# Kernel optimization log

Hardware: AMD Instinct MI355X
Metric: run time of the kernel (lower is better)

## Reference

```python
import jax, jax.numpy as jnp
import numpy as np

NUM_EMBEDDINGS = 1024
EMBEDDING_DIM = 256
COMMITMENT_COST = 0.25
DECAY = 0.99
EPSILON = 1e-05


def setup_inputs() -> dict:
    key = jax.random.key(0)
    k1, k2, k3 = jax.random.split(key, 3)
    z_e = jax.random.normal(k1, (32, 32, 32, EMBEDDING_DIM), dtype=jnp.float32)
    embedding = jax.random.normal(k2, (NUM_EMBEDDINGS, EMBEDDING_DIM), dtype=jnp.float32)
    ema_cluster_size = jnp.zeros((NUM_EMBEDDINGS,), dtype=jnp.float32)
    ema_w = jax.random.normal(k3, (NUM_EMBEDDINGS, EMBEDDING_DIM), dtype=jnp.float32)
    return {"z_e": z_e, "embedding": embedding,
            "ema_cluster_size": ema_cluster_size, "ema_w": ema_w}


def reference(z_e, embedding, ema_cluster_size, ema_w):
    K, D = embedding.shape
    flat = z_e.reshape(-1, D)  # [N, D]
    distances = (jnp.sum(flat * flat, axis=1, keepdims=True)
                 - 2.0 * (flat @ embedding.T)
                 + jnp.sum(embedding * embedding, axis=1))
    encoding_indices = jnp.argmin(distances, axis=1)  # [N]
    # one_hot @ embedding == gather of nearest codes
    z_q = embedding[encoding_indices].reshape(z_e.shape)

    # EMA codebook update (training branch, torch no_grad)
    counts = jax.ops.segment_sum(jnp.ones_like(encoding_indices, dtype=flat.dtype),
                                 encoding_indices, num_segments=K)  # encodings.sum(0)
    dw = jax.ops.segment_sum(flat, encoding_indices, num_segments=K)  # encodings.T @ flat
    new_cluster_size = DECAY * ema_cluster_size + (1.0 - DECAY) * counts
    new_ema_w = DECAY * ema_w + (1.0 - DECAY) * dw
    n = jnp.sum(new_cluster_size)
    cluster_size = (new_cluster_size + EPSILON) / (n + K * EPSILON) * n
    new_embedding = new_ema_w / cluster_size[:, None]

    codebook_loss = jnp.mean((z_q - jax.lax.stop_gradient(z_e)) ** 2)
    commitment_loss = COMMITMENT_COST * jnp.mean((z_e - jax.lax.stop_gradient(z_q)) ** 2)
    vq_loss = codebook_loss + commitment_loss
    z_q_st = z_e + jax.lax.stop_gradient(z_q - z_e)  # straight-through
    return (z_q_st, vq_loss, encoding_indices,
            new_embedding, new_cluster_size, new_ema_w)
```

## Files before the change

### kernel.cpp

```cpp
#include <hip/hip_runtime.h>

#define DECAY_F 0.99f
#define OMD_F   0.01f
#define EPS_F   1e-5f

typedef __attribute__((ext_vector_type(8)))  __bf16 bf16x8;
typedef __attribute__((ext_vector_type(16))) float  f32x16;

#define WSB_CNTI     0
#define WSB_LOSS     4096
#define WSB_DWACC    8192
#define WSB_CSUM     1056768
#define WSB_ENORM    1056832
#define WSB_IDX      1060928
#define WSB_EHI      1192000
#define WSB_ELO      1716288
#define WSB_SORT     2240576
#define WSB_CURS     2371648

#define OUT_ZQ    0
#define OUT_LOSS  8388608
#define OUT_IDX   8388609
#define OUT_EMB   8421377
#define OUT_CS    8683521
#define OUT_EMAW  8684545

__device__ __forceinline__ unsigned short f2bf(float x) {
    unsigned u = __builtin_bit_cast(unsigned, x);
    u += 0x7fffu + ((u >> 16) & 1u);
    return (unsigned short)(u >> 16);
}
__device__ __forceinline__ float bf2f(unsigned short h) {
    return __builtin_bit_cast(float, (unsigned)h << 16);
}
__device__ __forceinline__ void split8(const float4 a, const float4 b,
                                       uint4& hi, uint4& lo) {
    float f[8] = {a.x, a.y, a.z, a.w, b.x, b.y, b.z, b.w};
    unsigned short h[8], l[8];
    #pragma unroll
    for (int i = 0; i < 8; ++i) {
        h[i] = f2bf(f[i]);
        l[i] = f2bf(f[i] - bf2f(h[i]));
    }
    hi.x = (unsigned)h[0] | ((unsigned)h[1] << 16);
    hi.y = (unsigned)h[2] | ((unsigned)h[3] << 16);
    hi.z = (unsigned)h[4] | ((unsigned)h[5] << 16);
    hi.w = (unsigned)h[6] | ((unsigned)h[7] << 16);
    lo.x = (unsigned)l[0] | ((unsigned)l[1] << 16);
    lo.y = (unsigned)l[2] | ((unsigned)l[3] << 16);
    lo.z = (unsigned)l[4] | ((unsigned)l[5] << 16);
    lo.w = (unsigned)l[6] | ((unsigned)l[7] << 16);
}

__device__ __forceinline__ void load_lds16(const void* g, void* l) {
    __builtin_amdgcn_global_load_lds(
        (const __attribute__((address_space(1))) unsigned int*)g,
        (__attribute__((address_space(3))) unsigned int*)l, 16, 0, 0);
}

__global__ __launch_bounds__(256)
void esplit_enorm_kernel(const float* __restrict__ emb,
                         unsigned short* __restrict__ e_hi,
                         unsigned short* __restrict__ e_lo,
                         float* __restrict__ enorm,
                         float* __restrict__ dwacc,
                         int* __restrict__ cnt,
                         float* __restrict__ lossbuf) {
    const int tid = threadIdx.x, lane = tid & 63, wv = tid >> 6;
    const int gthread = blockIdx.x * 256 + tid;
    *(float4*)(dwacc + (size_t)gthread * 4) = make_float4(0.f, 0.f, 0.f, 0.f);
    if (gthread < 1024) cnt[gthread] = 0;
    if (gthread < 256)  lossbuf[gthread] = 0.f;

    const int k = blockIdx.x * 4 + wv;
    const float4 v = *(const float4*)(emb + (size_t)k * 256 + lane * 4);
    float f[4] = {v.x, v.y, v.z, v.w};
    unsigned short h[4], l[4];
    #pragma unroll
    for (int i = 0; i < 4; ++i) { h[i] = f2bf(f[i]); l[i] = f2bf(f[i] - bf2f(h[i])); }
    uint2 hi, lo;
    hi.x = (unsigned)h[0] | ((unsigned)h[1] << 16);
    hi.y = (unsigned)h[2] | ((unsigned)h[3] << 16);
    lo.x = (unsigned)l[0] | ((unsigned)l[1] << 16);
    lo.y = (unsigned)l[2] | ((unsigned)l[3] << 16);
    *(uint2*)(e_hi + (size_t)k * 256 + lane * 4) = hi;
    *(uint2*)(e_lo + (size_t)k * 256 + lane * 4) = lo;
    float s = v.x * v.x + v.y * v.y + v.z * v.z + v.w * v.w;
    #pragma unroll
    for (int off = 32; off > 0; off >>= 1) s += __shfl_down(s, off);
    if (lane == 0) enorm[k] = s;
}

__global__ __launch_bounds__(256, 2)
void argmin_kernel(const float* __restrict__ z,
                   const unsigned short* __restrict__ e_hi,
                   const unsigned short* __restrict__ e_lo,
                   const float* __restrict__ enorm,
                   const float* __restrict__ emb,
                   int* __restrict__ idx, float* __restrict__ idxf,
                   float* __restrict__ out_zq, int* __restrict__ cnt) {
    __shared__ unsigned short Ah[64 * 32], Al[64 * 32];
    __shared__ unsigned short Bh[256 * 32], Bl[256 * 32];

    const int tid  = threadIdx.x;
    const int lane = tid & 63;
    const int wv   = tid >> 6;
    const int l31  = lane & 31, lh = lane >> 5;
    const int row0 = blockIdx.x * 64;

    const int rA = tid >> 2, gA = tid & 3;
    const float* zA = z + (size_t)(row0 + rA) * 256 + gA * 8;
    const int offA = rA * 32 + ((gA ^ ((rA >> 1) & 3)) << 3);

    int gBoff[4], lBoff[4];
    #pragma unroll
    for (int i = 0; i < 4; ++i) {
        const int s = i * 256 + wv * 64 + lane;
        const int c = s >> 2, gp = s & 3;
        const int gl = gp ^ ((c >> 1) & 3);
        gBoff[i] = c * 256 + gl * 8;
        lBoff[i] = (i * 256 + wv * 64) * 8;
    }

    int offAf[2][2], offBf[2][2];
    #pragma unroll
    for (int i = 0; i < 2; ++i) {
        const int rt = i * 32 + l31;
        #pragma unroll
        for (int kk = 0; kk < 2; ++kk)
            offAf[i][kk] = rt * 32 + (((kk * 2 + lh) ^ ((rt >> 1) & 3)) << 3);
    }
    #pragma unroll
    for (int j = 0; j < 2; ++j) {
        const int cb = wv * 64 + j * 32 + l31;
        #pragma unroll
        for (int kk = 0; kk < 2; ++kk)
            offBf[j][kk] = cb * 32 + (((kk * 2 + lh) ^ ((cb >> 1) & 3)) << 3);
    }

    f32x16 acc[2][2];
    #pragma unroll
    for (int i = 0; i < 2; ++i)
        #pragma unroll
        for (int j = 0; j < 2; ++j) acc[i][j] = (f32x16)0.0f;

    float bestd[2][16];
    int   besti[2][16];
    #pragma unroll
    for (int i = 0; i < 2; ++i)
        #pragma unroll
        for (int r = 0; r < 16; ++r) { bestd[i][r] = 3.4e38f; besti[i][r] = 0; }

    float4 pA[2];
    auto prefA = [&](int kc_) {
        const int o = kc_ * 32;
        pA[0] = *(const float4*)(zA + o);
        pA[1] = *(const float4*)(zA + o + 4);
    };
    prefA(0);

    for (int csp = 0; csp < 4; ++csp) {
        const int ebase = csp * 65536;

        for (int kc = 0; kc < 8; ++kc) {
            __syncthreads();
            {
                uint4 h0, l0;
                split8(pA[0], pA[1], h0, l0);
                *(uint4*)(Ah + offA) = h0; *(uint4*)(Al + offA) = l0;
            }
            #pragma unroll
            for (int i = 0; i < 4; ++i) {
                load_lds16(e_hi + ebase + gBoff[i] + kc * 32, Bh + lBoff[i]);
                load_lds16(e_lo + ebase + gBoff[i] + kc * 32, Bl + lBoff[i]);
            }
            __syncthreads();
            if (kc < 7) prefA(kc + 1);
            else if (csp < 3) prefA(0);

            #pragma unroll
            for (int kk = 0; kk < 2; ++kk) {
                bf16x8 ah[2], al[2], bh[2], bl[2];
                #pragma unroll
                for (int i = 0; i < 2; ++i) {
                    ah[i] = __builtin_bit_cast(bf16x8, *(const uint4*)(Ah + offAf[i][kk]));
                    al[i] = __builtin_bit_cast(bf16x8, *(const uint4*)(Al + offAf[i][kk]));
                }
                #pragma unroll
                for (int j = 0; j < 2; ++j) {
                    bh[j] = __builtin_bit_cast(bf16x8, *(const uint4*)(Bh + offBf[j][kk]));
                    bl[j] = __builtin_bit_cast(bf16x8, *(const uint4*)(Bl + offBf[j][kk]));
                }
                #pragma unroll
                for (int j = 0; j < 2; ++j)
                    #pragma unroll
                    for (int i = 0; i < 2; ++i)
                        acc[i][j] = __builtin_amdgcn_mfma_f32_32x32x16_bf16(ah[i], bh[j], acc[i][j], 0, 0, 0);
                #pragma unroll
                for (int j = 0; j < 2; ++j)
                    #pragma unroll
                    for (int i = 0; i < 2; ++i)
                        acc[i][j] = __builtin_amdgcn_mfma_f32_32x32x16_bf16(al[i], bh[j], acc[i][j], 0, 0, 0);
                #pragma unroll
                for (int j = 0; j < 2; ++j)
                    #pragma unroll
                    for (int i = 0; i < 2; ++i)
                        acc[i][j] = __builtin_amdgcn_mfma_f32_32x32x16_bf16(ah[i], bl[j], acc[i][j], 0, 0, 0);
            }
        }

        #pragma unroll
        for (int j = 0; j < 2; ++j) {
            const int col = csp * 256 + wv * 64 + j * 32 + l31;
            const float en = enorm[col];
            #pragma unroll
            for (int i = 0; i < 2; ++i)
                #pragma unroll
                for (int r = 0; r < 16; ++r) {
                    const float d = fmaf(-2.0f, acc[i][j][r], en);
                    if (d < bestd[i][r] || (d == bestd[i][r] && col < besti[i][r])) {
                        bestd[i][r] = d; besti[i][r] = col;
                    }
                }
        }
        #pragma unroll
        for (int i = 0; i < 2; ++i)
            #pragma unroll
            for (int j = 0; j < 2; ++j) acc[i][j] = (f32x16)0.0f;
    }

    #pragma unroll
    for (int m = 1; m < 32; m <<= 1) {
        #pragma unroll
        for (int i = 0; i < 2; ++i)
            #pragma unroll
            for (int r = 0; r < 16; ++r) {
                const float od = __shfl_xor(bestd[i][r], m);
                const int   oi = __shfl_xor(besti[i][r], m);
                if (od < bestd[i][r] || (od == bestd[i][r] && oi < besti[i][r])) {
                    bestd[i][r] = od; besti[i][r] = oi;
                }
            }
    }

    __syncthreads();
    float* mg_d = (float*)Ah;
    int*   mg_i = (int*)Ah + 256;
    if (l31 == 0) {
        #pragma unroll
        for (int i = 0; i < 2; ++i)
            #pragma unroll
            for (int r = 0; r < 16; ++r) {
                const int rloc = i * 32 + (r & 3) + 8 * (r >> 2) + 4 * lh;
                mg_d[wv * 64 + rloc] = bestd[i][r];
                mg_i[wv * 64 + rloc] = besti[i][r];
            }
    }
    __syncthreads();
    if (tid < 64) {
        float d0 = mg_d[tid];
        int   i0 = mg_i[tid];
        #pragma unroll
        for (int w = 1; w < 4; ++w) {
            const float dw = mg_d[w * 64 + tid];
            const int   iw = mg_i[w * 64 + tid];
            if (dw < d0 || (dw == d0 && iw < i0)) { d0 = dw; i0 = iw; }
        }
        const int n = row0 + tid;
        idx[n] = i0; idxf[n] = (float)i0;
        atomicAdd(&cnt[i0], 1);
        mg_i[tid] = i0;
    }
    __syncthreads();

    #pragma unroll 4
    for (int r = 0; r < 16; ++r) {
        const int row = wv * 16 + r;
        const int code = mg_i[row];
        const float4 e4 = *(const float4*)(emb + (size_t)code * 256 + lane * 4);
        *(float4*)(out_zq + (size_t)(row0 + row) * 256 + lane * 4) = e4;
    }
}

__global__ __launch_bounds__(1024)
void scan_kernel(const float* __restrict__ ema_cs, const int* __restrict__ cnt,
                 float* __restrict__ out_cs, float* __restrict__ csum,
                 int* __restrict__ cursor) {
    __shared__ int   wtmp[16];
    __shared__ float wred[16];
    const int t = threadIdx.x, lane = t & 63, wv = t >> 6;
    const int c = cnt[t];
    const float f = DECAY_F * ema_cs[t] + OMD_F * (float)c;
    out_cs[t] = f;
    float fs = f;
    #pragma unroll
    for (int o = 32; o > 0; o >>= 1) fs += __shfl_down(fs, o);
    if (lane == 0) wred[wv] = fs;
    int v = c;
    #pragma unroll
    for (int o = 1; o < 64; o <<= 1) { const int u = __shfl_up(v, o); if (lane >= o) v += u; }
    if (lane == 63) wtmp[wv] = v;
    __syncthreads();
    if (t == 0) { float s2 = 0.f; for (int w = 0; w < 16; ++w) s2 += wred[w]; csum[0] = s2; }
    int wbase = 0;
    #pragma unroll
    for (int w = 0; w < 16; ++w) if (w < wv) wbase += wtmp[w];
    cursor[t] = wbase + v - c;
}

__global__ __launch_bounds__(256)
void scatter_kernel(const int* __restrict__ idx, int* __restrict__ cursor,
                    int* __restrict__ sorted) {
    const int n = blockIdx.x * 256 + threadIdx.x;
    const int k = idx[n];
    const int p = atomicAdd(&cursor[k], 1);
    sorted[p] = n;
}

__global__ __launch_bounds__(256)
void dw_kernel(const float* __restrict__ z, const float* __restrict__ emb,
               const float* __restrict__ enorm,
               const int* __restrict__ sorted, const int* __restrict__ idx,
               float* __restrict__ dwacc, float* __restrict__ lossbuf) {
    const int lane = threadIdx.x & 63;
    const int w    = blockIdx.x * 4 + (threadIdx.x >> 6);
    const int r0   = w * 16;
    const int srow = sorted[r0 + (lane & 15)];
    const int skey = idx[srow];

    float4 s = make_float4(0.f, 0.f, 0.f, 0.f);
    float sumsq = 0.f;
    int cntr = 0;
    int krun = __shfl(skey, 0);

    auto flush = [&](int k) {
        const float4 e = *(const float4*)(emb + (size_t)k * 256 + lane * 4);
        float val = sumsq - 2.0f * (e.x * s.x + e.y * s.y + e.z * s.z + e.w * s.w);
        #pragma unroll
        for (int off = 32; off > 0; off >>= 1) val += __shfl_down(val, off);
        if (lane == 0) atomicAdd(&lossbuf[k & 255], val + (float)cntr * enorm[k]);
        float* p = dwacc + (size_t)k * 256 + lane * 4;
        atomicAdd(p + 0, s.x); atomicAdd(p + 1, s.y);
        atomicAdd(p + 2, s.z); atomicAdd(p + 3, s.w);
    };

    #pragma unroll 8
    for (int j = 0; j < 16; ++j) {
        const int row = __shfl(srow, j);
        const int k   = __shfl(skey, j);
        if (k != krun) {
            flush(krun);
            s = make_float4(0.f, 0.f, 0.f, 0.f);
            sumsq = 0.f; cntr = 0; krun = k;
        }
        const float4 v = *(const float4*)(z + (size_t)row * 256 + lane * 4);
        s.x += v.x; s.y += v.y; s.z += v.z; s.w += v.w;
        sumsq += v.x * v.x + v.y * v.y + v.z * v.z + v.w * v.w;
        ++cntr;
    }
    flush(krun);
}

__global__ __launch_bounds__(256)
void update_w_kernel(const float* __restrict__ ema_w, const float* __restrict__ dwacc,
                     const float* __restrict__ out_cs, const float* __restrict__ csum,
                     const float* __restrict__ lossbuf,
                     float* __restrict__ out_emb, float* __restrict__ out_emaw,
                     float* __restrict__ out_loss) {
    __shared__ float red[256];
    const int t = threadIdx.x;
    if (blockIdx.x == 0) {
        red[t] = lossbuf[t]; __syncthreads();
        #pragma unroll
        for (int off = 128; off > 0; off >>= 1) {
            if (t < off) red[t] += red[t + off];
            __syncthreads();
        }
        if (t == 0) out_loss[0] = 1.25f * red[0] / 8388608.0f;
    }

    const int g = blockIdx.x * 256 + t;
    const int k = g >> 6;
    const float n_total = csum[0];
    const float cs = (out_cs[k] + EPS_F) / (n_total + 1024.0f * EPS_F) * n_total;

    const float4 w4 = *(const float4*)(ema_w + (size_t)g * 4);
    const float4 d4 = *(const float4*)(dwacc + (size_t)g * 4);
    float4 nw, ne;
    nw.x = DECAY_F * w4.x + OMD_F * d4.x;
    nw.y = DECAY_F * w4.y + OMD_F * d4.y;
    nw.z = DECAY_F * w4.z + OMD_F * d4.z;
    nw.w = DECAY_F * w4.w + OMD_F * d4.w;
    ne.x = nw.x / cs; ne.y = nw.y / cs; ne.z = nw.z / cs; ne.w = nw.w / cs;
    *(float4*)(out_emaw + (size_t)g * 4) = nw;
    *(float4*)(out_emb  + (size_t)g * 4) = ne;
}

extern "C" void kernel_launch(void* const* d_in, const int* in_sizes, int n_in,
                              void* d_out, int out_size, void* d_ws, size_t ws_size,
                              hipStream_t stream) {
    const float* z      = (const float*)d_in[0];
    const float* emb    = (const float*)d_in[1];
    const float* ema_cs = (const float*)d_in[2];
    const float* ema_w  = (const float*)d_in[3];

    float* out = (float*)d_out;
    char*  wsb = (char*)d_ws;

    int*            cnt     = (int*)(wsb + WSB_CNTI);
    float*          lossbuf = (float*)(wsb + WSB_LOSS);
    float*          dwacc   = (float*)(wsb + WSB_DWACC);
    float*          csum    = (float*)(wsb + WSB_CSUM);
    float*          enorm   = (float*)(wsb + WSB_ENORM);
    int*            idx     = (int*)(wsb + WSB_IDX);
    unsigned short* e_hi    = (unsigned short*)(wsb + WSB_EHI);
    unsigned short* e_lo    = (unsigned short*)(wsb + WSB_ELO);
    int*            sorted  = (int*)(wsb + WSB_SORT);
    int*            cursor  = (int*)(wsb + WSB_CURS);

    float* out_zq   = out + OUT_ZQ;
    float* out_loss = out + OUT_LOSS;
    float* out_idxf = out + OUT_IDX;
    float* out_emb  = out + OUT_EMB;
    float* out_cs   = out + OUT_CS;
    float* out_emaw = out + OUT_EMAW;

    esplit_enorm_kernel<<<256, 256, 0, stream>>>(emb, e_hi, e_lo, enorm,
                                                 dwacc, cnt, lossbuf);
    argmin_kernel<<<512, 256, 0, stream>>>(z, e_hi, e_lo, enorm, emb,
                                           idx, out_idxf, out_zq, cnt);
    scan_kernel<<<1, 1024, 0, stream>>>(ema_cs, cnt, out_cs, csum, cursor);
    scatter_kernel<<<128, 256, 0, stream>>>(idx, cursor, sorted);
    dw_kernel<<<512, 256, 0, stream>>>(z, emb, enorm, sorted, idx, dwacc, lossbuf);
    update_w_kernel<<<256, 256, 0, stream>>>(ema_w, dwacc, out_cs, csum, lossbuf,
                                             out_emb, out_emaw, out_loss);
}
```

Measured before the change: 226.7 us.

## Pre-swizzle codebook into MFMA fragment order and stream B from registers

The embedding split kernel now writes the bf16 hi/lo codebook in MFMA fragment-major order, so each wave can load its B fragments straight from global memory into registers with coalesced 16-byte loads. The whole 64x256 A tile is split once into LDS at kernel start, and the per-k-chunk barriers and LDS staging of B are removed. B loads are double-buffered in registers across steps. This drops the LDS traffic and the repeated __syncthreads, at the cost of more registers and no sharing of B across waves through LDS, since each wave now reads its own distinct slice.

```diff
diff --git a/kernel.cpp b/kernel.cpp
--- a/kernel.cpp
+++ b/kernel.cpp
@@ -52,12 +52,6 @@
     lo.w = (unsigned)l[6] | ((unsigned)l[7] << 16);
 }
 
-__device__ __forceinline__ void load_lds16(const void* g, void* l) {
-    __builtin_amdgcn_global_load_lds(
-        (const __attribute__((address_space(1))) unsigned int*)g,
-        (__attribute__((address_space(3))) unsigned int*)l, 16, 0, 0);
-}
-
 __global__ __launch_bounds__(256)
 void esplit_enorm_kernel(const float* __restrict__ emb,
                          unsigned short* __restrict__ e_hi,
@@ -68,23 +62,31 @@
                          float* __restrict__ lossbuf) {
     const int tid = threadIdx.x, lane = tid & 63, wv = tid >> 6;
     const int gthread = blockIdx.x * 256 + tid;
+
     *(float4*)(dwacc + (size_t)gthread * 4) = make_float4(0.f, 0.f, 0.f, 0.f);
     if (gthread < 1024) cnt[gthread] = 0;
     if (gthread < 256)  lossbuf[gthread] = 0.f;
 
+    if (gthread < 32768) {
+        const int F     = gthread;
+        const int chunk = F >> 6;
+        const int lh6   = (F >> 5) & 1;
+        const int l31f  = F & 31;
+        const int g     = chunk >> 4;
+        const int kc    = (chunk >> 1) & 7;
+        const int kk    = chunk & 1;
+        const int k     = g * 32 + l31f;
+        const int d0    = kc * 32 + (kk * 2 + lh6) * 8;
+        const float4 v0 = *(const float4*)(emb + (size_t)k * 256 + d0);
+        const float4 v1 = *(const float4*)(emb + (size_t)k * 256 + d0 + 4);
+        uint4 h, l;
+        split8(v0, v1, h, l);
+        *(uint4*)((char*)e_hi + (size_t)F * 16) = h;
+        *(uint4*)((char*)e_lo + (size_t)F * 16) = l;
+    }
+
     const int k = blockIdx.x * 4 + wv;
     const float4 v = *(const float4*)(emb + (size_t)k * 256 + lane * 4);
-    float f[4] = {v.x, v.y, v.z, v.w};
-    unsigned short h[4], l[4];
-    #pragma unroll
-    for (int i = 0; i < 4; ++i) { h[i] = f2bf(f[i]); l[i] = f2bf(f[i] - bf2f(h[i])); }
-    uint2 hi, lo;
-    hi.x = (unsigned)h[0] | ((unsigned)h[1] << 16);
-    hi.y = (unsigned)h[2] | ((unsigned)h[3] << 16);
-    lo.x = (unsigned)l[0] | ((unsigned)l[1] << 16);
-    lo.y = (unsigned)l[2] | ((unsigned)l[3] << 16);
-    *(uint2*)(e_hi + (size_t)k * 256 + lane * 4) = hi;
-    *(uint2*)(e_lo + (size_t)k * 256 + lane * 4) = lo;
     float s = v.x * v.x + v.y * v.y + v.z * v.z + v.w * v.w;
     #pragma unroll
     for (int off = 32; off > 0; off >>= 1) s += __shfl_down(s, off);
@@ -99,8 +101,7 @@
                    const float* __restrict__ emb,
                    int* __restrict__ idx, float* __restrict__ idxf,
                    float* __restrict__ out_zq, int* __restrict__ cnt) {
-    __shared__ unsigned short Ah[64 * 32], Al[64 * 32];
-    __shared__ unsigned short Bh[256 * 32], Bl[256 * 32];
+    __shared__ unsigned short Ah[32 * 512], Al[32 * 512];
 
     const int tid  = threadIdx.x;
     const int lane = tid & 63;
@@ -108,35 +109,20 @@
     const int l31  = lane & 31, lh = lane >> 5;
     const int row0 = blockIdx.x * 64;
 
-    const int rA = tid >> 2, gA = tid & 3;
-    const float* zA = z + (size_t)(row0 + rA) * 256 + gA * 8;
-    const int offA = rA * 32 + ((gA ^ ((rA >> 1) & 3)) << 3);
-
-    int gBoff[4], lBoff[4];
-    #pragma unroll
-    for (int i = 0; i < 4; ++i) {
-        const int s = i * 256 + wv * 64 + lane;
-        const int c = s >> 2, gp = s & 3;
-        const int gl = gp ^ ((c >> 1) & 3);
-        gBoff[i] = c * 256 + gl * 8;
-        lBoff[i] = (i * 256 + wv * 64) * 8;
-    }
-
-    int offAf[2][2], offBf[2][2];
-    #pragma unroll
-    for (int i = 0; i < 2; ++i) {
-        const int rt = i * 32 + l31;
-        #pragma unroll
-        for (int kk = 0; kk < 2; ++kk)
-            offAf[i][kk] = rt * 32 + (((kk * 2 + lh) ^ ((rt >> 1) & 3)) << 3);
-    }
-    #pragma unroll
-    for (int j = 0; j < 2; ++j) {
-        const int cb = wv * 64 + j * 32 + l31;
-        #pragma unroll
-        for (int kk = 0; kk < 2; ++kk)
-            offBf[j][kk] = cb * 32 + (((kk * 2 + lh) ^ ((cb >> 1) & 3)) << 3);
-    }
+    #pragma unroll
+    for (int c8 = 0; c8 < 8; ++c8) {
+        const int C  = wv * 8 + c8;
+        const int i  = C >> 4, kc = (C >> 1) & 7, kk = C & 1;
+        const int row = row0 + i * 32 + l31;
+        const int d0  = kc * 32 + (kk * 2 + lh) * 8;
+        const float4 v0 = *(const float4*)(z + (size_t)row * 256 + d0);
+        const float4 v1 = *(const float4*)(z + (size_t)row * 256 + d0 + 4);
+        uint4 h, l;
+        split8(v0, v1, h, l);
+        *(uint4*)((char*)Ah + (size_t)C * 1024 + lane * 16) = h;
+        *(uint4*)((char*)Al + (size_t)C * 1024 + lane * 16) = l;
+    }
+    __syncthreads();
 
     f32x16 acc[2][2];
     #pragma unroll
@@ -151,82 +137,72 @@
         #pragma unroll
         for (int r = 0; r < 16; ++r) { bestd[i][r] = 3.4e38f; besti[i][r] = 0; }
 
-    float4 pA[2];
-    auto prefA = [&](int kc_) {
-        const int o = kc_ * 32;
-        pA[0] = *(const float4*)(zA + o);
-        pA[1] = *(const float4*)(zA + o + 4);
+    uint4 b0h[4], b0l[4], b1h[4], b1l[4];
+    auto loadB = [&](int s, uint4* bh, uint4* bl) {
+        const int csp = s >> 3, kc = s & 7;
+        #pragma unroll
+        for (int j = 0; j < 2; ++j)
+            #pragma unroll
+            for (int kk = 0; kk < 2; ++kk) {
+                const int chunk = (csp * 8 + wv * 2 + j) * 16 + kc * 2 + kk;
+                bh[j * 2 + kk] = *(const uint4*)((const char*)e_hi + (size_t)chunk * 1024 + lane * 16);
+                bl[j * 2 + kk] = *(const uint4*)((const char*)e_lo + (size_t)chunk * 1024 + lane * 16);
+            }
     };
-    prefA(0);
-
-    for (int csp = 0; csp < 4; ++csp) {
-        const int ebase = csp * 65536;
-
-        for (int kc = 0; kc < 8; ++kc) {
-            __syncthreads();
-            {
-                uint4 h0, l0;
-                split8(pA[0], pA[1], h0, l0);
-                *(uint4*)(Ah + offA) = h0; *(uint4*)(Al + offA) = l0;
-            }
-            #pragma unroll
-            for (int i = 0; i < 4; ++i) {
-                load_lds16(e_hi + ebase + gBoff[i] + kc * 32, Bh + lBoff[i]);
-                load_lds16(e_lo + ebase + gBoff[i] + kc * 32, Bl + lBoff[i]);
-            }
-            __syncthreads();
-            if (kc < 7) prefA(kc + 1);
-            else if (csp < 3) prefA(0);
-
-            #pragma unroll
-            for (int kk = 0; kk < 2; ++kk) {
-                bf16x8 ah[2], al[2], bh[2], bl[2];
-                #pragma unroll
-                for (int i = 0; i < 2; ++i) {
-                    ah[i] = __builtin_bit_cast(bf16x8, *(const uint4*)(Ah + offAf[i][kk]));
-                    al[i] = __builtin_bit_cast(bf16x8, *(const uint4*)(Al + offAf[i][kk]));
-                }
+    auto compute = [&](int s, const uint4* bh4, const uint4* bl4) {
+        const int kc = s & 7;
+        #pragma unroll
+        for (int kk = 0; kk < 2; ++kk) {
+            bf16x8 bh[2], bl[2];
+            #pragma unroll
+            for (int j = 0; j < 2; ++j) {
+                bh[j] = __builtin_bit_cast(bf16x8, bh4[j * 2 + kk]);
+                bl[j] = __builtin_bit_cast(bf16x8, bl4[j * 2 + kk]);
+            }
+            #pragma unroll
+            for (int i = 0; i < 2; ++i) {
+                const int C = i * 16 + kc * 2 + kk;
+                const bf16x8 ah = __builtin_bit_cast(bf16x8,
+                    *(const uint4*)((const char*)Ah + (size_t)C * 1024 + lane * 16));
+                const bf16x8 al = __builtin_bit_cast(bf16x8,
+                    *(const uint4*)((const char*)Al + (size_t)C * 1024 + lane * 16));
                 #pragma unroll
                 for (int j = 0; j < 2; ++j) {
-                    bh[j] = __builtin_bit_cast(bf16x8, *(const uint4*)(Bh + offBf[j][kk]));
-                    bl[j] = __builtin_bit_cast(bf16x8, *(const uint4*)(Bl + offBf[j][kk]));
+                    acc[i][j] = __builtin_amdgcn_mfma_f32_32x32x16_bf16(ah, bh[j], acc[i][j], 0, 0, 0);
+                    acc[i][j] = __builtin_amdgcn_mfma_f32_32x32x16_bf16(al, bh[j], acc[i][j], 0, 0, 0);
+                    acc[i][j] = __builtin_amdgcn_mfma_f32_32x32x16_bf16(ah, bl[j], acc[i][j], 0, 0, 0);
                 }
+            }
+        }
+        if ((s & 7) == 7) {
+            const int csp = s >> 3;
+            #pragma unroll
+            for (int j = 0; j < 2; ++j) {
+                const int col = csp * 256 + wv * 64 + j * 32 + l31;
+                const float en = enorm[col];
                 #pragma unroll
-                for (int j = 0; j < 2; ++j)
+                for (int i = 0; i < 2; ++i)
                     #pragma unroll
-                    for (int i = 0; i < 2; ++i)
-                        acc[i][j] = __builtin_amdgcn_mfma_f32_32x32x16_bf16(ah[i], bh[j], acc[i][j], 0, 0, 0);
-                #pragma unroll
-                for (int j = 0; j < 2; ++j)
-                    #pragma unroll
-                    for (int i = 0; i < 2; ++i)
-                        acc[i][j] = __builtin_amdgcn_mfma_f32_32x32x16_bf16(al[i], bh[j], acc[i][j], 0, 0, 0);
-                #pragma unroll
-                for (int j = 0; j < 2; ++j)
-                    #pragma unroll
-                    for (int i = 0; i < 2; ++i)
-                        acc[i][j] = __builtin_amdgcn_mfma_f32_32x32x16_bf16(ah[i], bl[j], acc[i][j], 0, 0, 0);
-            }
-        }
-
-        #pragma unroll
-        for (int j = 0; j < 2; ++j) {
-            const int col = csp * 256 + wv * 64 + j * 32 + l31;
-            const float en = enorm[col];
+                    for (int r = 0; r < 16; ++r) {
+                        const float d = fmaf(-2.0f, acc[i][j][r], en);
+                        if (d < bestd[i][r] || (d == bestd[i][r] && col < besti[i][r])) {
+                            bestd[i][r] = d; besti[i][r] = col;
+                        }
+                    }
+            }
             #pragma unroll
             for (int i = 0; i < 2; ++i)
                 #pragma unroll
-                for (int r = 0; r < 16; ++r) {
-                    const float d = fmaf(-2.0f, acc[i][j][r], en);
-                    if (d < bestd[i][r] || (d == bestd[i][r] && col < besti[i][r])) {
-                        bestd[i][r] = d; besti[i][r] = col;
-                    }
-                }
+                for (int j = 0; j < 2; ++j) acc[i][j] = (f32x16)0.0f;
         }
-        #pragma unroll
-        for (int i = 0; i < 2; ++i)
-            #pragma unroll
-            for (int j = 0; j < 2; ++j) acc[i][j] = (f32x16)0.0f;
+    };
+
+    loadB(0, b0h, b0l);
+    for (int s = 0; s < 32; s += 2) {
+        loadB(s + 1, b1h, b1l);
+        compute(s, b0h, b0l);
+        if (s + 2 < 32) loadB(s + 2, b0h, b0l);
+        compute(s + 1, b1h, b1l);
     }
 
     #pragma unroll
```

Result: faster. 206.9 us (-8.7%).
